# Kernel optimization log

Hardware: AMD Instinct MI355X
Metric: run time of the kernel (lower is better)

## Reference

```python
import jax, jax.numpy as jnp
import numpy as np

NEG_SLOPE = 0.2  # HANConv default negative_slope
N_NODES = 100000
N_REL = 8
N_EDGES = 200000
N_LABEL = 131072
C_IN = 128
H1 = 128
H2 = 128


def _segment_softmax(logits, seg, num_segments):
    # PyG softmax(src, index): exp(src - max_per_seg) / (sum_per_seg + 1e-16)
    m = jax.ops.segment_max(logits, seg, num_segments=num_segments)
    m = jnp.where(jnp.isfinite(m), m, 0.0)  # empty segments -> 0
    e = jnp.exp(logits - m[seg])
    s = jax.ops.segment_sum(e, seg, num_segments=num_segments)
    return e / (s[seg] + 1e-16)


def _han_layer(x, edge_index, proj_w, proj_b, att_src, att_dst, q, klin_w, klin_b):
    # x: [N, Cin]; edge_index: [R, 2, E]; att_src/att_dst: [R, D]; klin_w: [D, D] (torch [out,in])
    N = x.shape[0]
    h = x @ proj_w + proj_b            # [N, D] shared projection for node type 'node'
    a_src = h @ att_src.T              # [N, R] per-node src attention logits
    a_dst = h @ att_dst.T              # [N, R]

    def per_rel(eidx, a_s, a_d):
        src, dst = eidx[0], eidx[1]
        alpha = jax.nn.leaky_relu(a_s[src] + a_d[dst], NEG_SLOPE)     # [E]
        alpha = _segment_softmax(alpha, dst, N)                        # softmax over in-neighbors
        out = jax.ops.segment_sum(alpha[:, None] * h[src], dst, num_segments=N)  # [N, D]
        return jax.nn.relu(out)        # HANConv applies relu per edge-type output

    outs = jax.vmap(per_rel, in_axes=(0, 1, 1))(edge_index, a_src, a_dst)  # [R, N, D]
    # semantic attention across edge types (group())
    score = jnp.einsum('d,rd->r', q, jnp.tanh(outs @ klin_w.T + klin_b).mean(axis=1))
    attn = jax.nn.softmax(score)       # [R]
    return jnp.einsum('r,rnd->nd', attn, outs)


def setup_inputs() -> dict:
    key = jax.random.key(0)
    ks = jax.random.split(key, 24)
    f32 = jnp.float32

    def lin_w(k, fin, fout):
        return (jax.random.normal(k, (fin, fout), f32) / np.sqrt(fin)).astype(f32)

    inp = {
        'x': jax.random.normal(ks[0], (N_NODES, C_IN), f32),
        'edge_index': jax.random.randint(ks[1], (N_REL, 2, N_EDGES), 0, N_NODES, jnp.int32),
        'edge_label_index': jax.random.randint(ks[2], (2, N_LABEL), 0, N_NODES, jnp.int32),
        # HANConv layer 1 params
        'w1': lin_w(ks[3], C_IN, H1), 'b1': jnp.zeros((H1,), f32),
        'asrc1': jax.random.normal(ks[4], (N_REL, H1), f32) / np.sqrt(H1),
        'adst1': jax.random.normal(ks[5], (N_REL, H1), f32) / np.sqrt(H1),
        'q1': jax.random.normal(ks[6], (H1,), f32) / np.sqrt(H1),
        'kw1': lin_w(ks[7], H1, H1).T, 'kb1': jnp.zeros((H1,), f32),
        # HANConv layer 2 params
        'w2': lin_w(ks[8], H1, H2), 'b2': jnp.zeros((H2,), f32),
        'asrc2': jax.random.normal(ks[9], (N_REL, H2), f32) / np.sqrt(H2),
        'adst2': jax.random.normal(ks[10], (N_REL, H2), f32) / np.sqrt(H2),
        'q2': jax.random.normal(ks[11], (H2,), f32) / np.sqrt(H2),
        'kw2': lin_w(ks[12], H2, H2).T, 'kb2': jnp.zeros((H2,), f32),
        # link-score head
        'post_w': lin_w(ks[13], H2, 2), 'post_b': jnp.zeros((2,), f32),
    }
    return inp


def reference(x, edge_index, edge_label_index,
              w1, b1, asrc1, adst1, q1, kw1, kb1,
              w2, b2, asrc2, adst2, q2, kw2, kb2,
              post_w, post_b):
    h = jax.nn.relu(_han_layer(x, edge_index, w1, b1, asrc1, adst1, q1, kw1, kb1))
    h = jax.nn.relu(_han_layer(h, edge_index, w2, b2, asrc2, adst2, q2, kw2, kb2))
    h_had = h[edge_label_index[0]] * h[edge_label_index[1]]   # [L, H2]
    logits = h_had @ post_w + post_b                          # [L, 2]
    return logits.sum(axis=-1)                                # [L]
```

## Files before the change

kernel.cpp:

```cpp
#include <hip/hip_runtime.h>

#define NN 100000
#define NR 8
#define NE 200000
#define NL 131072
#define NSEG (NR*NN)
#define NB_SCAN 782
#define NPAD (NB_SCAN*1024)

typedef __attribute__((ext_vector_type(8))) short short8;
typedef __attribute__((ext_vector_type(4))) float floatx4;

__device__ __forceinline__ unsigned short f2bf(float f) {
    unsigned u = __float_as_uint(f);
    unsigned r = (u + 0x7fff + ((u >> 16) & 1)) >> 16;
    return (unsigned short)r;
}
__device__ __forceinline__ float bf2f(unsigned short s) {
    return __uint_as_float(((unsigned)s) << 16);
}

__global__ void transpose128(const float* __restrict__ in, float* __restrict__ out) {
    int idx = blockIdx.x * 256 + threadIdx.x;
    int j = idx >> 7, k = idx & 127;
    out[idx] = in[k * 128 + j];
}

__global__ void cast_bf16(const float* __restrict__ src, unsigned short* __restrict__ dst) {
    size_t idx = ((size_t)blockIdx.x * 256 + threadIdx.x) * 4;
    float4 v = *(const float4*)(src + idx);
    ushort4 o;
    o.x = f2bf(v.x); o.y = f2bf(v.y); o.z = f2bf(v.z); o.w = f2bf(v.w);
    *(ushort4*)(dst + idx) = o;
}

__global__ void hist_kernel(const int* __restrict__ ei, int* __restrict__ counts) {
    int idx = blockIdx.x * 256 + threadIdx.x;
    if (idx >= NR * NE) return;
    int r = idx / NE, e = idx - r * NE;
    int dst = ei[(size_t)r * 2 * NE + NE + e];
    atomicAdd(&counts[r * NN + dst], 1);
}

__global__ __launch_bounds__(256) void scan_k1(const int* __restrict__ counts,
                                               int* __restrict__ rowptr,
                                               int* __restrict__ bsums) {
    __shared__ int wsum[4];
    int t = threadIdx.x, lane = t & 63, w = t >> 6;
    int base = blockIdx.x * 1024 + t * 4;
    int c0 = counts[base], c1 = counts[base + 1], c2 = counts[base + 2], c3 = counts[base + 3];
    int s = c0 + c1 + c2 + c3;
    int inc = s;
#pragma unroll
    for (int off = 1; off < 64; off <<= 1) { int v = __shfl_up(inc, off); if (lane >= off) inc += v; }
    if (lane == 63) wsum[w] = inc;
    __syncthreads();
    int wbase = 0;
    for (int k = 0; k < w; ++k) wbase += wsum[k];
    int ex = wbase + inc - s;
    rowptr[base]     = ex;
    rowptr[base + 1] = ex + c0;
    rowptr[base + 2] = ex + c0 + c1;
    rowptr[base + 3] = ex + c0 + c1 + c2;
    if (t == 255) bsums[blockIdx.x] = wbase + inc;
}

__global__ __launch_bounds__(256) void scan_k2(int* __restrict__ bsums, int nb) {
    __shared__ int wsum[4];
    __shared__ int carry_s;
    int t = threadIdx.x, lane = t & 63, w = t >> 6;
    if (t == 0) carry_s = 0;
    __syncthreads();
    for (int base = 0; base < nb; base += 256) {
        int i = base + t;
        int v = (i < nb) ? bsums[i] : 0;
        int inc = v;
#pragma unroll
        for (int off = 1; off < 64; off <<= 1) { int u = __shfl_up(inc, off); if (lane >= off) inc += u; }
        if (lane == 63) wsum[w] = inc;
        __syncthreads();
        int wbase = carry_s;
        for (int k = 0; k < w; ++k) wbase += wsum[k];
        if (i < nb) bsums[i] = wbase + inc - v;
        __syncthreads();
        if (t == 0) carry_s += wsum[0] + wsum[1] + wsum[2] + wsum[3];
        __syncthreads();
    }
}

__global__ void scan_k3(int* __restrict__ rowptr, const int* __restrict__ bsums) {
    int i = blockIdx.x * 256 + threadIdx.x;
    if (i <= NSEG) rowptr[i] += bsums[i >> 10];
}

__global__ void fill_kernel(const int* __restrict__ ei, const int* __restrict__ rowptr,
                            int* __restrict__ cursor, int* __restrict__ src_s) {
    int idx = blockIdx.x * 256 + threadIdx.x;
    if (idx >= NR * NE) return;
    int r = idx / NE, e = idx - r * NE;
    int src = ei[(size_t)r * 2 * NE + e];
    int dst = ei[(size_t)r * 2 * NE + NE + e];
    int g = r * NN + dst;
    int pos = rowptr[g] + atomicAdd(&cursor[g], 1);
    src_s[pos] = src;
}

__global__ __launch_bounds__(256, 3) void gemm_proj(
    const float* __restrict__ A, const float* __restrict__ B,
    const float* __restrict__ bias, float* __restrict__ out, int nrows)
{
    __shared__ float As[128][36];
    __shared__ float Bs[128][36];
    const int tid = threadIdx.x;
    const int row0 = blockIdx.x * 128;
    const int cg = tid & 15;
    const int nb = (tid >> 4) * 8;

    float acc[8][8];
#pragma unroll
    for (int i = 0; i < 8; ++i)
#pragma unroll
        for (int j = 0; j < 8; ++j) acc[i][j] = 0.f;

    for (int k0 = 0; k0 < 128; k0 += 32) {
#pragma unroll
        for (int i = 0; i < 4; ++i) {
            int fi = tid + i * 256;
            int rw = fi >> 3, kq = fi & 7;
            int n = row0 + rw;
            float4 v = make_float4(0.f, 0.f, 0.f, 0.f);
            if (n < nrows) v = *(const float4*)(A + (size_t)n * 128 + k0 + kq * 4);
            *(float4*)&As[rw][kq * 4] = v;
            float4 w = *(const float4*)(B + rw * 128 + k0 + kq * 4);
            *(float4*)&Bs[rw][kq * 4] = w;
        }
        __syncthreads();
#pragma unroll 2
        for (int kq = 0; kq < 8; ++kq) {
            float4 wv[8];
#pragma unroll
            for (int j = 0; j < 8; ++j) wv[j] = *(const float4*)&Bs[cg + 16 * j][kq * 4];
#pragma unroll
            for (int i = 0; i < 8; ++i) {
                float4 xv = *(const float4*)&As[nb + i][kq * 4];
#pragma unroll
                for (int j = 0; j < 8; ++j)
                    acc[i][j] += xv.x * wv[j].x + xv.y * wv[j].y
                               + xv.z * wv[j].z + xv.w * wv[j].w;
            }
        }
        __syncthreads();
    }
#pragma unroll
    for (int i = 0; i < 8; ++i) {
        int n = row0 + nb + i;
        if (n < nrows) {
#pragma unroll
            for (int j = 0; j < 8; ++j) {
                int d = cg + 16 * j;
                out[(size_t)n * 128 + d] = acc[i][j] + bias[d];
            }
        }
    }
}

__global__ __launch_bounds__(256) void fused_score2(
    const int* __restrict__ rowptr, const int* __restrict__ src_s,
    const float* __restrict__ alpha_s, const unsigned short* __restrict__ h16,
    const unsigned short* __restrict__ kw16, const float* __restrict__ kb,
    const float* __restrict__ q, float* __restrict__ score)
{
    __shared__ unsigned short Os[64][136];
    __shared__ float redbuf[4];
    const int t = threadIdx.x;
    const int r = blockIdx.y;
    const int row0 = blockIdx.x * 64;
    const int l = t & 15, ng = t >> 4;

#pragma unroll
    for (int pass = 0; pass < 4; ++pass) {
        int nl = pass * 16 + ng;
        int n = row0 + nl;
        float acc[8] = {0.f,0.f,0.f,0.f,0.f,0.f,0.f,0.f};
        if (n < NN) {
            int g = r * NN + n;
            int p0 = rowptr[g], p1 = rowptr[g + 1];
            for (int e = p0; e < p1; ++e) {
                float al = alpha_s[e];
                const unsigned short* hp = h16 + (size_t)src_s[e] * 128 + l * 8;
                ushort4 h0 = *(const ushort4*)hp;
                ushort4 h1 = *(const ushort4*)(hp + 4);
                acc[0] += al * bf2f(h0.x); acc[1] += al * bf2f(h0.y);
                acc[2] += al * bf2f(h0.z); acc[3] += al * bf2f(h0.w);
                acc[4] += al * bf2f(h1.x); acc[5] += al * bf2f(h1.y);
                acc[6] += al * bf2f(h1.z); acc[7] += al * bf2f(h1.w);
            }
        }
        unsigned short ov[8];
#pragma unroll
        for (int i = 0; i < 8; ++i) ov[i] = f2bf(fmaxf(acc[i], 0.f));
        *(short8*)&Os[nl][l * 8] = *(short8*)ov;
    }
    __syncthreads();

    const int wave = t >> 6, lane = t & 63;
    const int quad = lane >> 4, l16 = lane & 15;
    short8 a[4];
#pragma unroll
    for (int kc = 0; kc < 4; ++kc)
        a[kc] = *(const short8*)&Os[wave * 16 + l16][quad * 8 + kc * 32];

    float s = 0.f;
#pragma unroll
    for (int dt = 0; dt < 8; ++dt) {
        const unsigned short* brow = kw16 + (size_t)(dt * 16 + l16) * 128 + quad * 8;
        floatx4 accv = {0.f, 0.f, 0.f, 0.f};
#pragma unroll
        for (int kc = 0; kc < 4; ++kc) {
            short8 b = *(const short8*)(brow + kc * 32);
            accv = __builtin_amdgcn_mfma_f32_16x16x32_bf16(a[kc], b, accv, 0, 0, 0);
        }
        int d = dt * 16 + l16;
        float kbv = kb[d], qv = q[d];
#pragma unroll
        for (int reg = 0; reg < 4; ++reg) {
            int node = row0 + wave * 16 + quad * 4 + reg;
            if (node < NN) {
                float y = accv[reg] + kbv;
                float tn = 1.f - 2.f / (__expf(2.f * y) + 1.f);
                s += tn * qv;
            }
        }
    }
    for (int off = 32; off > 0; off >>= 1) s += __shfl_down(s, off);
    if (lane == 0) redbuf[wave] = s;
    __syncthreads();
    if (t == 0) atomicAdd(score + r, redbuf[0] + redbuf[1] + redbuf[2] + redbuf[3]);
}

__global__ __launch_bounds__(256) void att_kernel(
    const float* __restrict__ h, const float* __restrict__ asrc_w,
    const float* __restrict__ adst_w, float* __restrict__ a_src,
    float* __restrict__ a_dst, unsigned short* __restrict__ h16)
{
    __shared__ float hs[16][128];
    int n0 = blockIdx.x * 16;
#pragma unroll
    for (int i = 0; i < 2; ++i) {
        int fi = threadIdx.x + i * 256;
        int n = fi >> 5, kq = fi & 31;
        float4 v = make_float4(0.f, 0.f, 0.f, 0.f);
        if (n0 + n < NN) v = *(const float4*)(h + (size_t)(n0 + n) * 128 + kq * 4);
        *(float4*)&hs[n][kq * 4] = v;
    }
    __syncthreads();
    int n = threadIdx.x >> 4, rr = threadIdx.x & 15;
    int r = rr & 7; int isd = rr >> 3;
    const float* w = (isd ? adst_w : asrc_w) + r * 128;
    float acc = 0.f;
#pragma unroll
    for (int kq = 0; kq < 32; ++kq) {
        float4 hv = *(const float4*)&hs[n][kq * 4];
        float4 wv = ((const float4*)w)[kq];
        acc += hv.x * wv.x + hv.y * wv.y + hv.z * wv.z + hv.w * wv.w;
    }
    if (n0 + n < NN) (isd ? a_dst : a_src)[r * NN + n0 + n] = acc;

    int dq = rr * 8;
    if (n0 + n < NN) {
        unsigned short ov[8];
#pragma unroll
        for (int k = 0; k < 8; ++k) ov[k] = f2bf(hs[n][dq + k]);
        *(short8*)(h16 + (size_t)(n0 + n) * 128 + dq) = *(short8*)ov;
    }
}

__global__ void softmax_csr(const int* __restrict__ rowptr, const int* __restrict__ src_s,
                            const float* __restrict__ a_src, const float* __restrict__ a_dst,
                            float* __restrict__ alpha_s)
{
    int g = blockIdx.x * 256 + threadIdx.x;
    if (g >= NSEG) return;
    int p0 = rowptr[g], p1 = rowptr[g + 1];
    if (p0 == p1) return;
    int r = g / NN;
    float ad = a_dst[g];
    const float* as = a_src + (size_t)r * NN;
    float m = -1e30f;
    for (int i = p0; i < p1; ++i) {
        float l = as[src_s[i]] + ad;
        l = l > 0.f ? l : 0.2f * l;
        alpha_s[i] = l;
        m = fmaxf(m, l);
    }
    float s = 0.f;
    for (int i = p0; i < p1; ++i) {
        float e = __expf(alpha_s[i] - m);
        alpha_s[i] = e;
        s += e;
    }
    float inv = 1.f / (s + 1e-16f);
    for (int i = p0; i < p1; ++i) alpha_s[i] *= inv;
}

__global__ __launch_bounds__(256) void combine_csr(
    const int* __restrict__ rowptr, const int* __restrict__ src_s,
    const float* __restrict__ alpha_s, const float* __restrict__ h,
    const float* __restrict__ score, float* __restrict__ comb)
{
    __shared__ float attn[NR];
    __shared__ float lds[4][64][17];
    int t = threadIdx.x;
    if (t == 0) {
        float sc[NR]; float m = -1e30f;
        for (int r = 0; r < NR; ++r) { sc[r] = score[r] * (1.0f / NN); m = fmaxf(m, sc[r]); }
        float den = 0.f;
        for (int r = 0; r < NR; ++r) { sc[r] = __expf(sc[r] - m); den += sc[r]; }
        for (int r = 0; r < NR; ++r) attn[r] = sc[r] / den;
    }
    __syncthreads();

    int nl = t >> 6;
    int n = blockIdx.x * 4 + nl;
    int L = t & 63;
    int r = L >> 3;
    int d0 = (L & 7) * 16;
    float a[16];
#pragma unroll
    for (int i = 0; i < 16; ++i) a[i] = 0.f;
    {
        int g = r * NN + n;
        int p0 = rowptr[g], p1 = rowptr[g + 1];
        for (int e = p0; e < p1; ++e) {
            float al = alpha_s[e];
            const float* hp = h + (size_t)src_s[e] * 128 + d0;
            float4 v0 = *(const float4*)hp;
            float4 v1 = *(const float4*)(hp + 4);
            float4 v2 = *(const float4*)(hp + 8);
            float4 v3 = *(const float4*)(hp + 12);
            a[0]+=al*v0.x; a[1]+=al*v0.y; a[2]+=al*v0.z;  a[3]+=al*v0.w;
            a[4]+=al*v1.x; a[5]+=al*v1.y; a[6]+=al*v1.z;  a[7]+=al*v1.w;
            a[8]+=al*v2.x; a[9]+=al*v2.y; a[10]+=al*v2.z; a[11]+=al*v2.w;
            a[12]+=al*v3.x;a[13]+=al*v3.y;a[14]+=al*v3.z; a[15]+=al*v3.w;
        }
    }
    float w = attn[r];
    float* dst = &lds[nl][L][0];
#pragma unroll
    for (int i = 0; i < 16; ++i) dst[i] = w * fmaxf(a[i], 0.f);
    __syncthreads();

    int o = L >> 3, j = L & 7;
    float s0 = 0.f, s1 = 0.f;
#pragma unroll
    for (int rr = 0; rr < NR; ++rr) {
        s0 += lds[nl][rr * 8 + o][2 * j];
        s1 += lds[nl][rr * 8 + o][2 * j + 1];
    }
    *(float2*)(comb + (size_t)n * 128 + 2 * L) = make_float2(s0, s1);
}

__global__ __launch_bounds__(256) void head_kernel(
    const float* __restrict__ hfin, const int* __restrict__ eli,
    const float* __restrict__ pw, const float* __restrict__ pb,
    float* __restrict__ out)
{
    int t = threadIdx.x;
    int l = blockIdx.x * 4 + (t >> 6);
    int d0 = (t & 63) * 2;
    int a = eli[l], b = eli[NL + l];
    float2 ha = *(const float2*)(hfin + (size_t)a * 128 + d0);
    float2 hb = *(const float2*)(hfin + (size_t)b * 128 + d0);
    float w0 = pw[d0 * 2] + pw[d0 * 2 + 1];
    float w1 = pw[d0 * 2 + 2] + pw[d0 * 2 + 3];
    float v = ha.x * hb.x * w0 + ha.y * hb.y * w1;
    for (int off = 32; off > 0; off >>= 1) v += __shfl_down(v, off);
    if ((t & 63) == 0) out[l] = v + pb[0] + pb[1];
}

extern "C" void kernel_launch(void* const* d_in, const int* in_sizes, int n_in,
                              void* d_out, int out_size, void* d_ws, size_t ws_size,
                              hipStream_t stream)
{
    const float* x     = (const float*)d_in[0];
    const int*   ei    = (const int*)d_in[1];
    const int*   eli   = (const int*)d_in[2];
    const float* w1    = (const float*)d_in[3];
    const float* b1    = (const float*)d_in[4];
    const float* asrc1 = (const float*)d_in[5];
    const float* adst1 = (const float*)d_in[6];
    const float* q1    = (const float*)d_in[7];
    const float* kw1   = (const float*)d_in[8];
    const float* kb1   = (const float*)d_in[9];
    const float* w2    = (const float*)d_in[10];
    const float* b2    = (const float*)d_in[11];
    const float* asrc2 = (const float*)d_in[12];
    const float* adst2 = (const float*)d_in[13];
    const float* q2    = (const float*)d_in[14];
    const float* kw2   = (const float*)d_in[15];
    const float* kb2   = (const float*)d_in[16];
    const float* pw    = (const float*)d_in[17];
    const float* pb    = (const float*)d_in[18];
    float* out = (float*)d_out;

    float* ws      = (float*)d_ws;
    float* hA      = ws;
    float* hB      = ws + 12800000ull;
    float* a_src   = ws + 25600000ull;
    float* a_dst   = ws + 26400000ull;
    float* alpha_s = ws + 27200000ull;
    int*   src_s   = (int*)(ws + 28800000ull);
    int*   rowptr  = (int*)(ws + 30400000ull);
    int*   counts  = (int*)(ws + 31200768ull);
    int*   bsums   = (int*)(ws + 32001536ull);
    float* score   = ws + 32002560ull;
    float* wt      = ws + 32002624ull;
    unsigned short* kw16 = (unsigned short*)(ws + 32019008ull);
    unsigned short* h16 = (unsigned short*)hB;

    hipMemsetAsync(counts, 0, NPAD * sizeof(int), stream);
    hist_kernel<<<6250, 256, 0, stream>>>(ei, counts);
    scan_k1<<<NB_SCAN, 256, 0, stream>>>(counts, rowptr, bsums);
    scan_k2<<<1, 256, 0, stream>>>(bsums, NB_SCAN);
    scan_k3<<<3126, 256, 0, stream>>>(rowptr, bsums);
    hipMemsetAsync(counts, 0, NPAD * sizeof(int), stream);
    fill_kernel<<<6250, 256, 0, stream>>>(ei, rowptr, counts, src_s);

    for (int layer = 0; layer < 2; ++layer) {
        const float* Ain  = layer ? hB : x;
        const float* W    = layer ? w2 : w1;
        const float* bb   = layer ? b2 : b1;
        const float* as_w = layer ? asrc2 : asrc1;
        const float* ad_w = layer ? adst2 : adst1;
        const float* qq   = layer ? q2 : q1;
        const float* kw   = layer ? kw2 : kw1;
        const float* kb   = layer ? kb2 : kb1;

        transpose128<<<64, 256, 0, stream>>>(W, wt);
        gemm_proj<<<782, 256, 0, stream>>>(Ain, wt, bb, hA, NN);
        cast_bf16<<<16, 256, 0, stream>>>(kw, kw16);
        att_kernel<<<6250, 256, 0, stream>>>(hA, as_w, ad_w, a_src, a_dst, h16);
        softmax_csr<<<3125, 256, 0, stream>>>(rowptr, src_s, a_src, a_dst, alpha_s);
        hipMemsetAsync(score, 0, 64 * sizeof(float), stream);
        fused_score2<<<dim3(1563, NR), 256, 0, stream>>>(rowptr, src_s, alpha_s, h16,
                                                         kw16, kb, qq, score);
        combine_csr<<<25000, 256, 0, stream>>>(rowptr, src_s, alpha_s, hA, score, hB);
    }
    head_kernel<<<32768, 256, 0, stream>>>(hB, eli, pw, pb, out);
}
```

Measured before the change: 1.451 ms.

## Interleave edge source and alpha into int2 array; widen bf16 gather per lane

Source indices and softmax weights are stored interleaved as int2 so the aggregation kernels fetch both with a single 8-byte load rather than two separate arrays. In fused_score2 each lane now handles 16 bf16 features using two 16-byte loads, with 8 lanes per node and 2 passes instead of 16 lanes and 4 passes. This gives more independent edge loops per thread and wider memory transactions. Reciprocal intrinsics replace divisions in the tanh and the softmax normalisation, trading a little precision.

```diff
diff --git a/kernel.cpp b/kernel.cpp
--- a/kernel.cpp
+++ b/kernel.cpp
@@ -94,7 +94,7 @@
 }
 
 __global__ void fill_kernel(const int* __restrict__ ei, const int* __restrict__ rowptr,
-                            int* __restrict__ cursor, int* __restrict__ src_s) {
+                            int* __restrict__ cursor, int* __restrict__ es_raw) {
     int idx = blockIdx.x * 256 + threadIdx.x;
     if (idx >= NR * NE) return;
     int r = idx / NE, e = idx - r * NE;
@@ -102,7 +102,7 @@
     int dst = ei[(size_t)r * 2 * NE + NE + e];
     int g = r * NN + dst;
     int pos = rowptr[g] + atomicAdd(&cursor[g], 1);
-    src_s[pos] = src;
+    es_raw[2 * pos] = src;
 }
 
 __global__ __launch_bounds__(256, 3) void gemm_proj(
@@ -165,8 +165,8 @@
 }
 
 __global__ __launch_bounds__(256) void fused_score2(
-    const int* __restrict__ rowptr, const int* __restrict__ src_s,
-    const float* __restrict__ alpha_s, const unsigned short* __restrict__ h16,
+    const int* __restrict__ rowptr, const int2* __restrict__ es,
+    const unsigned short* __restrict__ h16,
     const unsigned short* __restrict__ kw16, const float* __restrict__ kb,
     const float* __restrict__ q, float* __restrict__ score)
 {
@@ -175,31 +175,35 @@
     const int t = threadIdx.x;
     const int r = blockIdx.y;
     const int row0 = blockIdx.x * 64;
-    const int l = t & 15, ng = t >> 4;
-
-#pragma unroll
-    for (int pass = 0; pass < 4; ++pass) {
-        int nl = pass * 16 + ng;
+    const int l = t & 7, ng = t >> 3;
+
+#pragma unroll
+    for (int pass = 0; pass < 2; ++pass) {
+        int nl = pass * 32 + ng;
         int n = row0 + nl;
-        float acc[8] = {0.f,0.f,0.f,0.f,0.f,0.f,0.f,0.f};
+        float acc[16];
+#pragma unroll
+        for (int i = 0; i < 16; ++i) acc[i] = 0.f;
         if (n < NN) {
             int g = r * NN + n;
             int p0 = rowptr[g], p1 = rowptr[g + 1];
             for (int e = p0; e < p1; ++e) {
-                float al = alpha_s[e];
-                const unsigned short* hp = h16 + (size_t)src_s[e] * 128 + l * 8;
-                ushort4 h0 = *(const ushort4*)hp;
-                ushort4 h1 = *(const ushort4*)(hp + 4);
-                acc[0] += al * bf2f(h0.x); acc[1] += al * bf2f(h0.y);
-                acc[2] += al * bf2f(h0.z); acc[3] += al * bf2f(h0.w);
-                acc[4] += al * bf2f(h1.x); acc[5] += al * bf2f(h1.y);
-                acc[6] += al * bf2f(h1.z); acc[7] += al * bf2f(h1.w);
+                int2 ep = es[e];
+                float al = __int_as_float(ep.y);
+                const unsigned short* hp = h16 + (size_t)ep.x * 128 + l * 16;
+                short8 h0 = *(const short8*)hp;
+                short8 h1 = *(const short8*)(hp + 8);
+#pragma unroll
+                for (int i = 0; i < 8; ++i) acc[i]     += al * bf2f((unsigned short)h0[i]);
+#pragma unroll
+                for (int i = 0; i < 8; ++i) acc[8 + i] += al * bf2f((unsigned short)h1[i]);
             }
         }
-        unsigned short ov[8];
-#pragma unroll
-        for (int i = 0; i < 8; ++i) ov[i] = f2bf(fmaxf(acc[i], 0.f));
-        *(short8*)&Os[nl][l * 8] = *(short8*)ov;
+        unsigned short ov[16];
+#pragma unroll
+        for (int i = 0; i < 16; ++i) ov[i] = f2bf(fmaxf(acc[i], 0.f));
+        *(short8*)&Os[nl][l * 16]     = *(short8*)&ov[0];
+        *(short8*)&Os[nl][l * 16 + 8] = *(short8*)&ov[8];
     }
     __syncthreads();
 
@@ -227,7 +231,8 @@
             int node = row0 + wave * 16 + quad * 4 + reg;
             if (node < NN) {
                 float y = accv[reg] + kbv;
-                float tn = 1.f - 2.f / (__expf(2.f * y) + 1.f);
+                float e2 = __expf(2.f * y);
+                float tn = 1.f - 2.f * __builtin_amdgcn_rcpf(e2 + 1.f);
                 s += tn * qv;
             }
         }
@@ -275,9 +280,8 @@
     }
 }
 
-__global__ void softmax_csr(const int* __restrict__ rowptr, const int* __restrict__ src_s,
-                            const float* __restrict__ a_src, const float* __restrict__ a_dst,
-                            float* __restrict__ alpha_s)
+__global__ void softmax_csr(const int* __restrict__ rowptr, int2* __restrict__ es,
+                            const float* __restrict__ a_src, const float* __restrict__ a_dst)
 {
     int g = blockIdx.x * 256 + threadIdx.x;
     if (g >= NSEG) return;
@@ -288,25 +292,26 @@
     const float* as = a_src + (size_t)r * NN;
     float m = -1e30f;
     for (int i = p0; i < p1; ++i) {
-        float l = as[src_s[i]] + ad;
+        float l = as[es[i].x] + ad;
         l = l > 0.f ? l : 0.2f * l;
-        alpha_s[i] = l;
+        es[i].y = __float_as_int(l);
         m = fmaxf(m, l);
     }
     float s = 0.f;
     for (int i = p0; i < p1; ++i) {
-        float e = __expf(alpha_s[i] - m);
-        alpha_s[i] = e;
+        float e = __expf(__int_as_float(es[i].y) - m);
+        es[i].y = __float_as_int(e);
         s += e;
     }
-    float inv = 1.f / (s + 1e-16f);
-    for (int i = p0; i < p1; ++i) alpha_s[i] *= inv;
+    float inv = __builtin_amdgcn_rcpf(s + 1e-16f);
+    for (int i = p0; i < p1; ++i)
+        es[i].y = __float_as_int(__int_as_float(es[i].y) * inv);
 }
 
 __global__ __launch_bounds__(256) void combine_csr(
-    const int* __restrict__ rowptr, const int* __restrict__ src_s,
-    const float* __restrict__ alpha_s, const float* __restrict__ h,
-    const float* __restrict__ score, float* __restrict__ comb)
+    const int* __restrict__ rowptr, const int2* __restrict__ es,
+    const float* __restrict__ h, const float* __restrict__ score,
+    float* __restrict__ comb)
 {
     __shared__ float attn[NR];
     __shared__ float lds[4][64][17];
@@ -332,8 +337,9 @@
         int g = r * NN + n;
         int p0 = rowptr[g], p1 = rowptr[g + 1];
         for (int e = p0; e < p1; ++e) {
-            float al = alpha_s[e];
-            const float* hp = h + (size_t)src_s[e] * 128 + d0;
+            int2 ep = es[e];
+            float al = __int_as_float(ep.y);
+            const float* hp = h + (size_t)ep.x * 128 + d0;
             float4 v0 = *(const float4*)hp;
             float4 v1 = *(const float4*)(hp + 4);
             float4 v2 = *(const float4*)(hp + 8);
@@ -408,8 +414,7 @@
     float* hB      = ws + 12800000ull;
     float* a_src   = ws + 25600000ull;
     float* a_dst   = ws + 26400000ull;
-    float* alpha_s = ws + 27200000ull;
-    int*   src_s   = (int*)(ws + 28800000ull);
+    int2*  es      = (int2*)(ws + 27200000ull);
     int*   rowptr  = (int*)(ws + 30400000ull);
     int*   counts  = (int*)(ws + 31200768ull);
     int*   bsums   = (int*)(ws + 32001536ull);
@@ -424,7 +429,7 @@
     scan_k2<<<1, 256, 0, stream>>>(bsums, NB_SCAN);
     scan_k3<<<3126, 256, 0, stream>>>(rowptr, bsums);
     hipMemsetAsync(counts, 0, NPAD * sizeof(int), stream);
-    fill_kernel<<<6250, 256, 0, stream>>>(ei, rowptr, counts, src_s);
+    fill_kernel<<<6250, 256, 0, stream>>>(ei, rowptr, counts, (int*)es);
 
     for (int layer = 0; layer < 2; ++layer) {
         const float* Ain  = layer ? hB : x;
@@ -440,11 +445,11 @@
         gemm_proj<<<782, 256, 0, stream>>>(Ain, wt, bb, hA, NN);
         cast_bf16<<<16, 256, 0, stream>>>(kw, kw16);
         att_kernel<<<6250, 256, 0, stream>>>(hA, as_w, ad_w, a_src, a_dst, h16);
-        softmax_csr<<<3125, 256, 0, stream>>>(rowptr, src_s, a_src, a_dst, alpha_s);
+        softmax_csr<<<3125, 256, 0, stream>>>(rowptr, es, a_src, a_dst);
         hipMemsetAsync(score, 0, 64 * sizeof(float), stream);
-        fused_score2<<<dim3(1563, NR), 256, 0, stream>>>(rowptr, src_s, alpha_s, h16,
+        fused_score2<<<dim3(1563, NR), 256, 0, stream>>>(rowptr, es, h16,
                                                          kw16, kb, qq, score);
-        combine_csr<<<25000, 256, 0, stream>>>(rowptr, src_s, alpha_s, hA, score, hB);
+        combine_csr<<<25000, 256, 0, stream>>>(rowptr, es, hA, score, hB);
     }
     head_kernel<<<32768, 256, 0, stream>>>(hB, eli, pw, pb, out);
 }
```

Result: no change. 1.430 ms (-1.4%).
